# Kernel tuning notes

Hardware: AMD Instinct MI355X
Metric: run time of the kernel (lower is better)

Reference implementation:

```python
import jax, jax.numpy as jnp
import numpy as np

D = 256      # d_model
NH = 8       # num heads
L = 2        # encoder layers
FF = 512     # dim_feedforward
WS = 2       # HiLo window_size
HD = D // NH # head dim = 32
LH = 4       # lofi heads (alpha=0.5)
HH = 4       # hifi heads
LD = LH * HD # 128
HDIM = HH * HD  # 128
SCALE = HD ** -0.5


def _ln(x, g, b):
    m = jnp.mean(x, -1, keepdims=True)
    v = jnp.mean((x - m) ** 2, -1, keepdims=True)
    return (x - m) / jnp.sqrt(v + 1e-5) * g + b


def _hilo(x, H, Wlq, Wlkv, Wlp, blp, Whqkv, Whp, bhp):
    N, B, C = x.shape
    x = x.reshape(B, H, N // H, C)  # faithful to torch: pure reshape, no permute
    Bc, Hh, Ww, Cc = x.shape
    hg, wg = Hh // WS, Ww // WS
    tg, n = hg * wg, WS * WS
    # ---- hifi: local windowed attention ----
    xg = x.reshape(Bc, hg, WS, wg, WS, Cc).swapaxes(2, 3).reshape(Bc, tg, n, Cc)
    qkv = (xg @ Whqkv).reshape(Bc, tg, n, 3, HH, HD)
    qkv = jnp.transpose(qkv, (3, 0, 1, 4, 2, 5))  # (3, B, tg, heads, n, hd)
    q, k, v = qkv[0], qkv[1], qkv[2]
    a = jax.nn.softmax((q @ jnp.swapaxes(k, -2, -1)) * SCALE, axis=-1)
    o = (a @ v).swapaxes(2, 3).reshape(Bc, hg, wg, WS, WS, HDIM)
    o = o.swapaxes(2, 3).reshape(Bc, Hh, Ww, HDIM)
    hi = o @ Whp + bhp
    # ---- lofi: full queries vs avg-pooled kv ----
    q = (x @ Wlq).reshape(Bc, Hh * Ww, LH, HD).transpose(0, 2, 1, 3)
    xp = x.reshape(Bc, hg, WS, wg, WS, Cc).mean(axis=(2, 4)).reshape(Bc, tg, Cc)
    kv = (xp @ Wlkv).reshape(Bc, tg, 2, LH, HD).transpose(2, 0, 3, 1, 4)
    k, v = kv[0], kv[1]
    a = jax.nn.softmax((q @ jnp.swapaxes(k, -2, -1)) * SCALE, axis=-1)
    lo = (a @ v).swapaxes(1, 2).reshape(Bc, Hh, Ww, LD) @ Wlp + blp
    return jnp.concatenate([hi, lo], axis=-1).reshape(N, B, C)


def setup_inputs() -> dict:
    key = jax.random.key(0)
    ks = jax.random.split(key, 10)
    w = lambda k, s: jax.random.normal(k, s, jnp.float32) * 0.02
    N, B = 128, 1024
    return {
        "tgt": jax.random.normal(ks[0], (N, B, D), jnp.float32),
        "Wlq": w(ks[1], (L, D, LD)),
        "Wlkv": w(ks[2], (L, D, 2 * LD)),
        "Wlp": w(ks[3], (L, LD, LD)),
        "blp": jnp.zeros((L, LD), jnp.float32),
        "Whqkv": w(ks[4], (L, D, 3 * HDIM)),
        "Whp": w(ks[5], (L, HDIM, HDIM)),
        "bhp": jnp.zeros((L, HDIM), jnp.float32),
        "W1": w(ks[6], (L, D, FF)),
        "b1": jnp.zeros((L, FF), jnp.float32),
        "W2": w(ks[7], (L, FF, D)),
        "b2": jnp.zeros((L, D), jnp.float32),
        "ln1_g": jnp.ones((L, D), jnp.float32),
        "ln1_b": jnp.zeros((L, D), jnp.float32),
        "ln2_g": jnp.ones((L, D), jnp.float32),
        "ln2_b": jnp.zeros((L, D), jnp.float32),
        "lnf_g": jnp.ones((D,), jnp.float32),
        "lnf_b": jnp.zeros((D,), jnp.float32),
        "enc_win_h": 8,
    }


def reference(tgt, Wlq, Wlkv, Wlp, blp, Whqkv, Whp, bhp, W1, b1, W2, b2,
              ln1_g, ln1_b, ln2_g, ln2_b, lnf_g, lnf_b, enc_win_h):
    out = tgt
    for i in range(L):
        a = _hilo(out, enc_win_h, Wlq[i], Wlkv[i], Wlp[i], blp[i], Whqkv[i], Whp[i], bhp[i])
        out = _ln(out + a, ln1_g[i], ln1_b[i])
        f = jax.nn.relu(out @ W1[i] + b1[i]) @ W2[i] + b2[i]
        out = _ln(out + f, ln2_g[i], ln2_b[i])
    out = _ln(out, lnf_g, lnf_b)
    return out[None]  # (1, N, B, C), matching output.unsqueeze(0)
```

## Files before the change

kernel.cpp:

```cpp
#include <hip/hip_runtime.h>
#include <hip/hip_bf16.h>


#define RT 131072ull
#define ATT_SCALE 0.17677669529663687f

typedef float f32x4 __attribute__((ext_vector_type(4)));
typedef __bf16 bf16x8 __attribute__((ext_vector_type(8)));
typedef unsigned short u16x8 __attribute__((ext_vector_type(8)));
typedef unsigned short u16x4 __attribute__((ext_vector_type(4)));

__device__ __forceinline__ unsigned short f2bf(float f) {
    unsigned int u = __float_as_uint(f);
    return (unsigned short)((u + 0x7FFFu + ((u >> 16) & 1u)) >> 16);
}
__device__ __forceinline__ float bf2f(unsigned short s) {
    return __uint_as_float(((unsigned int)s) << 16);
}
__device__ __forceinline__ void gload16(const void* g, void* l) {
    __builtin_amdgcn_global_load_lds(
        (const __attribute__((address_space(1))) unsigned int*)g,
        (__attribute__((address_space(3))) unsigned int*)l, 16, 0, 0);
}

__global__ __launch_bounds__(256) void wprep(const float* __restrict__ src,
                                             unsigned short* __restrict__ dst,
                                             int K, int N)
{
    __shared__ unsigned short t[32][33];
    int l = blockIdx.z;
    const float* s = src + (size_t)l * K * N;
    unsigned short* d = dst + (size_t)l * K * N;
    int r = threadIdx.x >> 3, c4 = (threadIdx.x & 7) * 4;
    int kb = blockIdx.x * 32, nb = blockIdx.y * 32;
    f32x4 v = *(const f32x4*)(s + (size_t)(kb + r) * N + nb + c4);
    #pragma unroll
    for (int j = 0; j < 4; ++j) t[c4 + j][r] = f2bf(v[j]);
    __syncthreads();
    u16x4 o;
    #pragma unroll
    for (int j = 0; j < 4; ++j) o[j] = t[r][c4 + j];
    *(u16x4*)(d + (size_t)(nb + r) * K + kb + c4) = o;
}

__global__ __launch_bounds__(256) void cvt_bf16(const float* __restrict__ src,
                                                unsigned short* __restrict__ dst)
{
    size_t i = ((size_t)blockIdx.x * 256 + threadIdx.x) * 8;
    f32x4 a = *(const f32x4*)(src + i);
    f32x4 b = *(const f32x4*)(src + i + 4);
    u16x8 t;
    #pragma unroll
    for (int j = 0; j < 4; ++j) { t[j] = f2bf(a[j]); t[4 + j] = f2bf(b[j]); }
    *(u16x8*)(dst + i) = t;
}

template<int MT, int NT, int KS>
__device__ __forceinline__ void mfma_gemm(const char* As, int astride, int am0,
    const unsigned short* __restrict__ BT, int ldbk, int koff,
    int lr, int lk, f32x4 (&acc)[MT][NT])
{
    #pragma unroll
    for (int s = 0; s < KS; ++s) {
        bf16x8 bfr[NT];
        #pragma unroll
        for (int nt = 0; nt < NT; ++nt)
            bfr[nt] = *(const bf16x8*)(BT + (size_t)(nt * 16 + lr) * ldbk + koff + s * 32 + lk * 8);
        #pragma unroll
        for (int mt = 0; mt < MT; ++mt) {
            int row = am0 + mt * 16 + lr;
            bf16x8 afr = *(const bf16x8*)(As + ((row * astride + s * 64 + lk * 16) ^ ((row & 7) << 4)));
            #pragma unroll
            for (int nt = 0; nt < NT; ++nt)
                acc[mt][nt] = __builtin_amdgcn_mfma_f32_16x16x32_bf16(afr, bfr[nt], acc[mt][nt], 0, 0, 0);
        }
    }
}

template<int MT, int NT, bool RELU>
__device__ __forceinline__ void store_lds(char* Ds, int dstride, int dm0, int dn0,
    const float* bias, int lr, int lk, f32x4 (&acc)[MT][NT])
{
    #pragma unroll
    for (int nt = 0; nt < NT; ++nt) {
        float bv = bias ? bias[nt * 16 + lr] : 0.0f;
        #pragma unroll
        for (int mt = 0; mt < MT; ++mt) {
            #pragma unroll
            for (int j = 0; j < 4; ++j) {
                int row = dm0 + mt * 16 + lk * 4 + j;
                int col = dn0 + nt * 16 + lr;
                float v = acc[mt][nt][j] + bv;
                if (RELU) v = fmaxf(v, 0.0f);
                *(unsigned short*)(Ds + ((row * dstride + col * 2) ^ ((row & 7) << 4))) = f2bf(v);
            }
        }
    }
}

template<int BN, bool BIAS, bool RELU>
__global__ __launch_bounds__(256) void gemm_bb(
    const unsigned short* __restrict__ A, int lda,
    const unsigned short* __restrict__ BT,
    const float* __restrict__ bias,
    unsigned short* __restrict__ C, int ldc, int K)
{
    constexpr int NT = BN / 32;
    __shared__ __align__(16) char As[128 * 128];
    __shared__ __align__(16) char Bs[BN * 128];

    const int tid = threadIdx.x;
    const size_t m0 = (size_t)blockIdx.x * 128;
    const int n0 = blockIdx.y * BN;
    const int w = tid >> 6, l = tid & 63;
    const int lr = l & 15, lk = l >> 4;
    const int wm = w >> 1, wn = w & 1;
    const int wb16 = (tid & ~63) * 16;

    f32x4 acc[4][NT] = {};

    for (int k0 = 0; k0 < K; k0 += 64) {
        #pragma unroll
        for (int i = 0; i < 4; ++i) {
            int cid = tid + i * 256, row = cid >> 3, kc = (cid & 7) ^ (row & 7);
            gload16(A + (m0 + row) * lda + k0 + kc * 8, As + i * 4096 + wb16);
        }
        #pragma unroll
        for (int i = 0; i < BN / 32; ++i) {
            int fid = tid + i * 256, row = fid >> 3, kc = (fid & 7) ^ (row & 7);
            gload16(BT + (size_t)(n0 + row) * K + k0 + kc * 8, Bs + i * 4096 + wb16);
        }
        __syncthreads();
        #pragma unroll
        for (int s = 0; s < 2; ++s) {
            bf16x8 bfr[NT];
            #pragma unroll
            for (int nt = 0; nt < NT; ++nt) {
                int r = wn * (BN / 2) + nt * 16 + lr;
                bfr[nt] = *(const bf16x8*)(Bs + ((r * 128 + s * 64 + lk * 16) ^ ((r & 7) << 4)));
            }
            #pragma unroll
            for (int mt = 0; mt < 4; ++mt) {
                int r = wm * 64 + mt * 16 + lr;
                bf16x8 afr = *(const bf16x8*)(As + ((r * 128 + s * 64 + lk * 16) ^ ((r & 7) << 4)));
                #pragma unroll
                for (int nt = 0; nt < NT; ++nt)
                    acc[mt][nt] = __builtin_amdgcn_mfma_f32_16x16x32_bf16(afr, bfr[nt], acc[mt][nt], 0, 0, 0);
            }
        }
        __syncthreads();
    }
    #pragma unroll
    for (int nt = 0; nt < NT; ++nt) {
        int col = n0 + wn * (BN / 2) + nt * 16 + lr;
        float bv = BIAS ? bias[col] : 0.0f;
        #pragma unroll
        for (int mt = 0; mt < 4; ++mt) {
            #pragma unroll
            for (int j = 0; j < 4; ++j) {
                size_t row = m0 + (size_t)(wm * 64 + mt * 16 + lk * 4 + j);
                float v = acc[mt][nt][j] + bv;
                if (RELU) v = fmaxf(v, 0.0f);
                C[row * ldc + col] = f2bf(v);
            }
        }
    }
}

__global__ __launch_bounds__(256) void hilo_ln(
    const unsigned short* __restrict__ os,
    const unsigned short* __restrict__ los,
    const unsigned short* __restrict__ x,
    const unsigned short* __restrict__ tWhp,
    const unsigned short* __restrict__ tWlp,
    const float* __restrict__ bhp, const float* __restrict__ blp,
    const float* __restrict__ g, const float* __restrict__ b,
    unsigned short* __restrict__ xout)
{
    __shared__ __align__(16) char sb[32768];
    char* Ao = sb;
    char* Al = sb + 16384;

    const int tid = threadIdx.x;
    const int w = tid >> 6, l = tid & 63;
    const int lr = l & 15, lk = l >> 4;
    const int wb16 = (tid & ~63) * 16;
    const size_t r0 = (size_t)blockIdx.x * 64;

    #pragma unroll
    for (int i = 0; i < 4; ++i) {
        int cid = tid + i * 256, row = cid >> 4, kc = (cid & 15) ^ (row & 7);
        gload16(os + (r0 + row) * 128 + kc * 8, Ao + i * 4096 + wb16);
        gload16(los + (r0 + row) * 128 + kc * 8, Al + i * 4096 + wb16);
    }
    __syncthreads();

    {
        const char* At = (w < 2) ? Ao : Al;
        const unsigned short* BTw = (w < 2) ? tWhp + (size_t)(w * 64) * 128
                                            : tWlp + (size_t)((w - 2) * 64) * 128;
        const float* biasw = (w < 2) ? bhp + w * 64 : blp + (w - 2) * 64;
        f32x4 acc[4][4] = {};
        mfma_gemm<4, 4, 4>(At, 256, 0, BTw, 128, 0, lr, lk, acc);
        __syncthreads();
        store_lds<4, 4, false>(sb, 512, 0, w * 64, biasw, lr, lk, acc);
    }
    __syncthreads();

    {
        int lrow = tid >> 2, c0 = (tid & 3) * 64;
        int xo = lrow * 512, sw = (lrow & 7) << 4;
        const unsigned short* xp = x + (r0 + lrow) * 256 + c0;
        float v[64];
        #pragma unroll
        for (int c = 0; c < 8; ++c) {
            u16x8 tr = *(const u16x8*)(sb + ((xo + c0 * 2 + c * 16) ^ sw));
            u16x8 tx = *(const u16x8*)(xp + c * 8);
            #pragma unroll
            for (int j = 0; j < 8; ++j) v[c * 8 + j] = bf2f(tx[j]) + bf2f(tr[j]);
        }
        float s = 0.0f, sq = 0.0f;
        #pragma unroll
        for (int j = 0; j < 64; ++j) { s += v[j]; sq += v[j] * v[j]; }
        s += __shfl_xor(s, 1); s += __shfl_xor(s, 2);
        sq += __shfl_xor(sq, 1); sq += __shfl_xor(sq, 2);
        float mean = s * (1.0f / 256.0f);
        float rstd = rsqrtf(sq * (1.0f / 256.0f) - mean * mean + 1e-5f);
        unsigned short* op = xout + (r0 + lrow) * 256 + c0;
        #pragma unroll
        for (int c = 0; c < 8; ++c) {
            u16x8 t;
            #pragma unroll
            for (int j = 0; j < 8; ++j)
                t[j] = f2bf((v[c * 8 + j] - mean) * rstd * g[c0 + c * 8 + j] + b[c0 + c * 8 + j]);
            *(u16x8*)(op + c * 8) = t;
        }
    }
}

__global__ __launch_bounds__(256) void hifi_attn(const unsigned short* __restrict__ qkv,
                                                 unsigned short* __restrict__ os)
{
    int t = blockIdx.x * 256 + threadIdx.x;
    int wdw = t >> 4, h = (t >> 2) & 3, qi = t & 3;
    int bc = wdw >> 5, tw = wdw & 31;
    int rbase = bc * 128 + (tw >> 3) * 32 + (tw & 7) * 2;
    int qrow = rbase + ((qi >> 1) << 4) + (qi & 1);

    const unsigned short* qp = qkv + (size_t)qrow * 384 + h * 32;
    float q[32];
    #pragma unroll
    for (int c = 0; c < 4; ++c) {
        u16x8 v = *(const u16x8*)(qp + c * 8);
        #pragma unroll
        for (int j = 0; j < 8; ++j) q[c * 8 + j] = bf2f(v[j]);
    }
    float s4[4];
    #pragma unroll
    for (int j = 0; j < 4; ++j) {
        int kr = rbase + ((j >> 1) << 4) + (j & 1);
        const unsigned short* kp = qkv + (size_t)kr * 384 + 128 + h * 32;
        float d = 0.0f;
        #pragma unroll
        for (int c = 0; c < 4; ++c) {
            u16x8 v = *(const u16x8*)(kp + c * 8);
            #pragma unroll
            for (int jj = 0; jj < 8; ++jj) d += q[c * 8 + jj] * bf2f(v[jj]);
        }
        s4[j] = d * ATT_SCALE;
    }
    float mx = fmaxf(fmaxf(s4[0], s4[1]), fmaxf(s4[2], s4[3]));
    float den = 0.0f;
    #pragma unroll
    for (int j = 0; j < 4; ++j) { s4[j] = __expf(s4[j] - mx); den += s4[j]; }
    float inv = 1.0f / den;

    float o[32];
    #pragma unroll
    for (int i = 0; i < 32; ++i) o[i] = 0.0f;
    #pragma unroll
    for (int j = 0; j < 4; ++j) {
        int vr = rbase + ((j >> 1) << 4) + (j & 1);
        const unsigned short* vp = qkv + (size_t)vr * 384 + 256 + h * 32;
        float a = s4[j] * inv;
        #pragma unroll
        for (int c = 0; c < 4; ++c) {
            u16x8 v = *(const u16x8*)(vp + c * 8);
            #pragma unroll
            for (int jj = 0; jj < 8; ++jj) o[c * 8 + jj] += a * bf2f(v[jj]);
        }
    }
    unsigned short* op = os + (size_t)qrow * 128 + h * 32;
    #pragma unroll
    for (int c = 0; c < 4; ++c) {
        u16x8 v;
        #pragma unroll
        for (int j = 0; j < 8; ++j) v[j] = f2bf(o[c * 8 + j]);
        *(u16x8*)(op + c * 8) = v;
    }
}

__global__ __launch_bounds__(256) void pool_k(const unsigned short* __restrict__ x,
                                              unsigned short* __restrict__ xp)
{
    int id = blockIdx.x * 256 + threadIdx.x;
    int p = id >> 5, c8 = (id & 31) * 8;
    int bc = p >> 5, tw = p & 31;
    int rbase = bc * 128 + (tw >> 3) * 32 + (tw & 7) * 2;
    const unsigned short* x0 = x + (size_t)rbase * 256 + c8;
    float a[8] = {};
    const int offs[4] = {0, 256, 16 * 256, 17 * 256};
    #pragma unroll
    for (int r = 0; r < 4; ++r) {
        u16x8 v = *(const u16x8*)(x0 + offs[r]);
        #pragma unroll
        for (int j = 0; j < 8; ++j) a[j] += bf2f(v[j]);
    }
    u16x8 o;
    #pragma unroll
    for (int j = 0; j < 8; ++j) o[j] = f2bf(a[j] * 0.25f);
    *(u16x8*)(xp + (size_t)p * 256 + c8) = o;
}

__global__ __launch_bounds__(128) void lofi_attn(const unsigned short* __restrict__ qb,
                                                 const unsigned short* __restrict__ kvb,
                                                 unsigned short* __restrict__ ob)
{
    __shared__ float ks[32][36];
    __shared__ float vs[32][36];
    int bc = blockIdx.x >> 2, h = blockIdx.x & 3;
    int tid = threadIdx.x;

    #pragma unroll
    for (int i = 0; i < 2; ++i) {
        int fid = tid + i * 128;
        int row = fid >> 3, cc = (fid & 7) * 4;
        const unsigned short* kp = kvb + (size_t)(bc * 32 + row) * 256 + h * 32 + cc;
        u16x4 kk = *(const u16x4*)kp;
        u16x4 vv = *(const u16x4*)(kp + 128);
        #pragma unroll
        for (int j = 0; j < 4; ++j) { ks[row][cc + j] = bf2f(kk[j]); vs[row][cc + j] = bf2f(vv[j]); }
    }

    const unsigned short* qp = qb + (size_t)(bc * 128 + tid) * 128 + h * 32;
    float q[32];
    #pragma unroll
    for (int c = 0; c < 4; ++c) {
        u16x8 v = *(const u16x8*)(qp + c * 8);
        #pragma unroll
        for (int j = 0; j < 8; ++j) q[c * 8 + j] = bf2f(v[j]);
    }
    __syncthreads();

    float sc[32];
    #pragma unroll
    for (int tk = 0; tk < 32; ++tk) {
        float d = 0.0f;
        #pragma unroll
        for (int i = 0; i < 32; ++i) d += q[i] * ks[tk][i];
        sc[tk] = d * ATT_SCALE;
    }
    float mx = -1e30f;
    #pragma unroll
    for (int tk = 0; tk < 32; ++tk) mx = fmaxf(mx, sc[tk]);
    float den = 0.0f;
    #pragma unroll
    for (int tk = 0; tk < 32; ++tk) { sc[tk] = __expf(sc[tk] - mx); den += sc[tk]; }
    float inv = 1.0f / den;

    float o[32];
    #pragma unroll
    for (int i = 0; i < 32; ++i) o[i] = 0.0f;
    #pragma unroll
    for (int tk = 0; tk < 32; ++tk) {
        float a = sc[tk];
        #pragma unroll
        for (int i = 0; i < 32; ++i) o[i] += a * vs[tk][i];
    }
    unsigned short* op = ob + (size_t)(bc * 128 + tid) * 128 + h * 32;
    #pragma unroll
    for (int c = 0; c < 4; ++c) {
        u16x8 v;
        #pragma unroll
        for (int j = 0; j < 8; ++j) v[j] = f2bf(o[c * 8 + j] * inv);
        *(u16x8*)(op + c * 8) = v;
    }
}

template<int MODE>
__global__ __launch_bounds__(256) void addln(
    const unsigned short* __restrict__ x,
    const unsigned short* __restrict__ r1,
    const float* __restrict__ g, const float* __restrict__ b,
    const float* __restrict__ g2, const float* __restrict__ b2,
    unsigned short* __restrict__ xout, float* __restrict__ fout)
{
    size_t row = (size_t)blockIdx.x * 4 + (threadIdx.x >> 6);
    int l = threadIdx.x & 63;
    u16x4 xv = *(const u16x4*)(x + row * 256 + l * 4);
    u16x4 rv = *(const u16x4*)(r1 + row * 256 + l * 4);
    f32x4 v;
    #pragma unroll
    for (int j = 0; j < 4; ++j) v[j] = bf2f(xv[j]) + bf2f(rv[j]);
    float s = v[0] + v[1] + v[2] + v[3];
    float sq = v[0] * v[0] + v[1] * v[1] + v[2] * v[2] + v[3] * v[3];
    #pragma unroll
    for (int off = 32; off > 0; off >>= 1) { s += __shfl_xor(s, off); sq += __shfl_xor(sq, off); }
    float mean = s * (1.0f / 256.0f);
    float rstd = rsqrtf(sq * (1.0f / 256.0f) - mean * mean + 1e-5f);
    f32x4 gv = *(const f32x4*)(g + l * 4);
    f32x4 bv = *(const f32x4*)(b + l * 4);
    f32x4 o;
    #pragma unroll
    for (int j = 0; j < 4; ++j) o[j] = (v[j] - mean) * rstd * gv[j] + bv[j];
    if (MODE == 2) {
        float s2 = o[0] + o[1] + o[2] + o[3];
        float sq2 = o[0] * o[0] + o[1] * o[1] + o[2] * o[2] + o[3] * o[3];
        #pragma unroll
        for (int off = 32; off > 0; off >>= 1) { s2 += __shfl_xor(s2, off); sq2 += __shfl_xor(sq2, off); }
        float mean2 = s2 * (1.0f / 256.0f);
        float rstd2 = rsqrtf(sq2 * (1.0f / 256.0f) - mean2 * mean2 + 1e-5f);
        f32x4 g2v = *(const f32x4*)(g2 + l * 4);
        f32x4 b2v = *(const f32x4*)(b2 + l * 4);
        f32x4 f;
        #pragma unroll
        for (int j = 0; j < 4; ++j) f[j] = (o[j] - mean2) * rstd2 * g2v[j] + b2v[j];
        *(f32x4*)(fout + row * 256 + l * 4) = f;
    } else {
        u16x4 t;
        #pragma unroll
        for (int j = 0; j < 4; ++j) t[j] = f2bf(o[j]);
        *(u16x4*)(xout + row * 256 + l * 4) = t;
    }
}

extern "C" void kernel_launch(void* const* d_in, const int* in_sizes, int n_in,
                              void* d_out, int out_size, void* d_ws, size_t ws_size,
                              hipStream_t stream)
{
    (void)in_sizes; (void)n_in; (void)out_size; (void)ws_size;
    const float* tgt   = (const float*)d_in[0];
    const float* Wlq   = (const float*)d_in[1];
    const float* Wlkv  = (const float*)d_in[2];
    const float* Wlp   = (const float*)d_in[3];
    const float* blp   = (const float*)d_in[4];
    const float* Whqkv = (const float*)d_in[5];
    const float* Whp   = (const float*)d_in[6];
    const float* bhp   = (const float*)d_in[7];
    const float* W1    = (const float*)d_in[8];
    const float* b1    = (const float*)d_in[9];
    const float* W2    = (const float*)d_in[10];
    const float* b2    = (const float*)d_in[11];
    const float* ln1g  = (const float*)d_in[12];
    const float* ln1b  = (const float*)d_in[13];
    const float* ln2g  = (const float*)d_in[14];
    const float* ln2b  = (const float*)d_in[15];
    const float* lnfg  = (const float*)d_in[16];
    const float* lnfb  = (const float*)d_in[17];

    unsigned short* wsu = (unsigned short*)d_ws;
    unsigned short* tWhqkv = wsu;
    unsigned short* tWhp   = wsu + 196608;
    unsigned short* tWlq   = wsu + 229376;
    unsigned short* tWlkv  = wsu + 294912;
    unsigned short* tWlp   = wsu + 425984;
    unsigned short* tW1    = wsu + 458752;
    unsigned short* tW2    = wsu + 720896;
    unsigned short* x    = wsu + 983040;
    unsigned short* qkv  = x + RT * 256;
    unsigned short* f    = qkv;
    unsigned short* los  = qkv + RT * 256;
    unsigned short* os   = qkv + RT * 384;
    unsigned short* qb   = os;
    unsigned short* xp   = os + RT * 128;
    unsigned short* kv   = xp + 32768ull * 256;
    unsigned short* hbuf = kv + 32768ull * 256;

    wprep<<<dim3(8, 12, 2), 256, 0, stream>>>(Whqkv, tWhqkv, 256, 384);
    wprep<<<dim3(4,  4, 2), 256, 0, stream>>>(Whp,   tWhp,   128, 128);
    wprep<<<dim3(8,  4, 2), 256, 0, stream>>>(Wlq,   tWlq,   256, 128);
    wprep<<<dim3(8,  8, 2), 256, 0, stream>>>(Wlkv,  tWlkv,  256, 256);
    wprep<<<dim3(4,  4, 2), 256, 0, stream>>>(Wlp,   tWlp,   128, 128);
    wprep<<<dim3(8, 16, 2), 256, 0, stream>>>(W1,    tW1,    256, 512);
    wprep<<<dim3(16, 8, 2), 256, 0, stream>>>(W2,    tW2,    512, 256);

    cvt_bf16<<<16384, 256, 0, stream>>>(tgt, x);

    for (int li = 0; li < 2; ++li) {
        gemm_bb<128, false, false><<<dim3(1024, 3), 256, 0, stream>>>(
            x, 256, tWhqkv + (size_t)li * 98304, nullptr, qkv, 384, 256);
        hifi_attn<<<2048, 256, 0, stream>>>(qkv, os);
        gemm_bb<128, false, false><<<dim3(1024, 1), 256, 0, stream>>>(
            x, 256, tWlq + (size_t)li * 32768, nullptr, hbuf, 128, 256);
        pool_k<<<4096, 256, 0, stream>>>(x, xp);
        gemm_bb<128, false, false><<<dim3(256, 2), 256, 0, stream>>>(
            xp, 256, tWlkv + (size_t)li * 65536, nullptr, kv, 256, 256);
        lofi_attn<<<4096, 128, 0, stream>>>(hbuf, kv, los);
        hilo_ln<<<2048, 256, 0, stream>>>(
            os, los, x, tWhp + (size_t)li * 16384, tWlp + (size_t)li * 16384,
            bhp + li * 128, blp + li * 128, ln1g + li * 256, ln1b + li * 256, x);
        gemm_bb<128, true, true><<<dim3(1024, 4), 256, 0, stream>>>(
            x, 256, tW1 + (size_t)li * 131072, b1 + li * 512, hbuf, 512, 256);
        gemm_bb<128, true, false><<<dim3(1024, 2), 256, 0, stream>>>(
            hbuf, 512, tW2 + (size_t)li * 131072, b2 + li * 256, f, 256, 512);
        if (li == 0) {
            addln<1><<<32768, 256, 0, stream>>>(x, f, ln2g, ln2b,
                                                nullptr, nullptr, x, nullptr);
        } else {
            addln<2><<<32768, 256, 0, stream>>>(x, f, ln2g + 256, ln2b + 256,
                                                lnfg, lnfb, nullptr, (float*)d_out);
        }
    }
}
```

Before: 967.6 us.

## Double-buffer GEMM LDS tiles and fuse hifi QKV with lofi Q projection

Converts the bf16 GEMM to double-buffered LDS, issuing the next K-tile's async global-to-LDS loads before computing the current tile, so memory latency overlaps MFMA work. It also concatenates the Whqkv and Wlq weights into one 512-wide matrix, so a single GEMM produces both the hifi QKV and the lofi Q. The attention kernels then read from the wider 512-stride buffer. LDS use doubles, which may lower occupancy, and the buffer layout is reshuffled.

```diff
diff --git a/kernel.cpp b/kernel.cpp
--- a/kernel.cpp
+++ b/kernel.cpp
@@ -25,12 +25,12 @@
 
 __global__ __launch_bounds__(256) void wprep(const float* __restrict__ src,
                                              unsigned short* __restrict__ dst,
-                                             int K, int N)
+                                             int K, int N, int ldd)
 {
     __shared__ unsigned short t[32][33];
     int l = blockIdx.z;
     const float* s = src + (size_t)l * K * N;
-    unsigned short* d = dst + (size_t)l * K * N;
+    unsigned short* d = dst + (size_t)l * ldd;
     int r = threadIdx.x >> 3, c4 = (threadIdx.x & 7) * 4;
     int kb = blockIdx.x * 32, nb = blockIdx.y * 32;
     f32x4 v = *(const f32x4*)(s + (size_t)(kb + r) * N + nb + c4);
@@ -99,15 +99,15 @@
 }
 
 template<int BN, bool BIAS, bool RELU>
-__global__ __launch_bounds__(256) void gemm_bb(
+__global__ __launch_bounds__(256) void gemm_db(
     const unsigned short* __restrict__ A, int lda,
     const unsigned short* __restrict__ BT,
     const float* __restrict__ bias,
     unsigned short* __restrict__ C, int ldc, int K)
 {
     constexpr int NT = BN / 32;
-    __shared__ __align__(16) char As[128 * 128];
-    __shared__ __align__(16) char Bs[BN * 128];
+    __shared__ __align__(16) char As[2][128 * 128];
+    __shared__ __align__(16) char Bs[2][BN * 128];
 
     const int tid = threadIdx.x;
     const size_t m0 = (size_t)blockIdx.x * 128;
@@ -118,31 +118,39 @@
     const int wb16 = (tid & ~63) * 16;
 
     f32x4 acc[4][NT] = {};
-
-    for (int k0 = 0; k0 < K; k0 += 64) {
+    const int nk = K >> 6;
+
+    auto stage = [&](int b, int k0) {
         #pragma unroll
         for (int i = 0; i < 4; ++i) {
             int cid = tid + i * 256, row = cid >> 3, kc = (cid & 7) ^ (row & 7);
-            gload16(A + (m0 + row) * lda + k0 + kc * 8, As + i * 4096 + wb16);
+            gload16(A + (m0 + row) * lda + k0 + kc * 8, As[b] + i * 4096 + wb16);
         }
         #pragma unroll
         for (int i = 0; i < BN / 32; ++i) {
             int fid = tid + i * 256, row = fid >> 3, kc = (fid & 7) ^ (row & 7);
-            gload16(BT + (size_t)(n0 + row) * K + k0 + kc * 8, Bs + i * 4096 + wb16);
-        }
-        __syncthreads();
+            gload16(BT + (size_t)(n0 + row) * K + k0 + kc * 8, Bs[b] + i * 4096 + wb16);
+        }
+    };
+
+    stage(0, 0);
+    __syncthreads();
+    for (int t = 0; t < nk; ++t) {
+        if (t + 1 < nk) stage((t + 1) & 1, (t + 1) << 6);
+        const char* Ab = As[t & 1];
+        const char* Bb = Bs[t & 1];
         #pragma unroll
         for (int s = 0; s < 2; ++s) {
             bf16x8 bfr[NT];
             #pragma unroll
             for (int nt = 0; nt < NT; ++nt) {
                 int r = wn * (BN / 2) + nt * 16 + lr;
-                bfr[nt] = *(const bf16x8*)(Bs + ((r * 128 + s * 64 + lk * 16) ^ ((r & 7) << 4)));
+                bfr[nt] = *(const bf16x8*)(Bb + ((r * 128 + s * 64 + lk * 16) ^ ((r & 7) << 4)));
             }
             #pragma unroll
             for (int mt = 0; mt < 4; ++mt) {
                 int r = wm * 64 + mt * 16 + lr;
-                bf16x8 afr = *(const bf16x8*)(As + ((r * 128 + s * 64 + lk * 16) ^ ((r & 7) << 4)));
+                bf16x8 afr = *(const bf16x8*)(Ab + ((r * 128 + s * 64 + lk * 16) ^ ((r & 7) << 4)));
                 #pragma unroll
                 for (int nt = 0; nt < NT; ++nt)
                     acc[mt][nt] = __builtin_amdgcn_mfma_f32_16x16x32_bf16(afr, bfr[nt], acc[mt][nt], 0, 0, 0);
@@ -247,7 +255,7 @@
     int rbase = bc * 128 + (tw >> 3) * 32 + (tw & 7) * 2;
     int qrow = rbase + ((qi >> 1) << 4) + (qi & 1);
 
-    const unsigned short* qp = qkv + (size_t)qrow * 384 + h * 32;
+    const unsigned short* qp = qkv + (size_t)qrow * 512 + h * 32;
     float q[32];
     #pragma unroll
     for (int c = 0; c < 4; ++c) {
@@ -259,7 +267,7 @@
     #pragma unroll
     for (int j = 0; j < 4; ++j) {
         int kr = rbase + ((j >> 1) << 4) + (j & 1);
-        const unsigned short* kp = qkv + (size_t)kr * 384 + 128 + h * 32;
+        const unsigned short* kp = qkv + (size_t)kr * 512 + 128 + h * 32;
         float d = 0.0f;
         #pragma unroll
         for (int c = 0; c < 4; ++c) {
@@ -281,7 +289,7 @@
     #pragma unroll
     for (int j = 0; j < 4; ++j) {
         int vr = rbase + ((j >> 1) << 4) + (j & 1);
-        const unsigned short* vp = qkv + (size_t)vr * 384 + 256 + h * 32;
+        const unsigned short* vp = qkv + (size_t)vr * 512 + 256 + h * 32;
         float a = s4[j] * inv;
         #pragma unroll
         for (int c = 0; c < 4; ++c) {
@@ -323,6 +331,7 @@
 }
 
 __global__ __launch_bounds__(128) void lofi_attn(const unsigned short* __restrict__ qb,
+                                                 int ldq,
                                                  const unsigned short* __restrict__ kvb,
                                                  unsigned short* __restrict__ ob)
 {
@@ -342,7 +351,7 @@
         for (int j = 0; j < 4; ++j) { ks[row][cc + j] = bf2f(kk[j]); vs[row][cc + j] = bf2f(vv[j]); }
     }
 
-    const unsigned short* qp = qb + (size_t)(bc * 128 + tid) * 128 + h * 32;
+    const unsigned short* qp = qb + (size_t)(bc * 128 + tid) * ldq + h * 32;
     float q[32];
     #pragma unroll
     for (int c = 0; c < 4; ++c) {
@@ -459,49 +468,45 @@
     const float* lnfb  = (const float*)d_in[17];
 
     unsigned short* wsu = (unsigned short*)d_ws;
-    unsigned short* tWhqkv = wsu;
-    unsigned short* tWhp   = wsu + 196608;
-    unsigned short* tWlq   = wsu + 229376;
+    unsigned short* tQ     = wsu;
+    unsigned short* tWhp   = wsu + 262144;
     unsigned short* tWlkv  = wsu + 294912;
     unsigned short* tWlp   = wsu + 425984;
     unsigned short* tW1    = wsu + 458752;
     unsigned short* tW2    = wsu + 720896;
-    unsigned short* x    = wsu + 983040;
-    unsigned short* qkv  = x + RT * 256;
-    unsigned short* f    = qkv;
-    unsigned short* los  = qkv + RT * 256;
-    unsigned short* os   = qkv + RT * 384;
-    unsigned short* qb   = os;
-    unsigned short* xp   = os + RT * 128;
-    unsigned short* kv   = xp + 32768ull * 256;
-    unsigned short* hbuf = kv + 32768ull * 256;
-
-    wprep<<<dim3(8, 12, 2), 256, 0, stream>>>(Whqkv, tWhqkv, 256, 384);
-    wprep<<<dim3(4,  4, 2), 256, 0, stream>>>(Whp,   tWhp,   128, 128);
-    wprep<<<dim3(8,  4, 2), 256, 0, stream>>>(Wlq,   tWlq,   256, 128);
-    wprep<<<dim3(8,  8, 2), 256, 0, stream>>>(Wlkv,  tWlkv,  256, 256);
-    wprep<<<dim3(4,  4, 2), 256, 0, stream>>>(Wlp,   tWlp,   128, 128);
-    wprep<<<dim3(8, 16, 2), 256, 0, stream>>>(W1,    tW1,    256, 512);
-    wprep<<<dim3(16, 8, 2), 256, 0, stream>>>(W2,    tW2,    512, 256);
+    unsigned short* x      = wsu + 983040;
+    unsigned short* qkv2   = x + RT * 256;
+    unsigned short* f      = qkv2;
+    unsigned short* xp     = qkv2 + RT * 512;
+    unsigned short* kv     = xp + 32768ull * 256;
+    unsigned short* hbuf   = kv + 32768ull * 256;
+    unsigned short* los    = hbuf;
+    unsigned short* os     = hbuf + RT * 128;
+
+    wprep<<<dim3(8, 12, 2), 256, 0, stream>>>(Whqkv, tQ, 256, 384, 131072);
+    wprep<<<dim3(8,  4, 2), 256, 0, stream>>>(Wlq, tQ + 98304, 256, 128, 131072);
+    wprep<<<dim3(4,  4, 2), 256, 0, stream>>>(Whp,  tWhp,  128, 128, 16384);
+    wprep<<<dim3(8,  8, 2), 256, 0, stream>>>(Wlkv, tWlkv, 256, 256, 65536);
+    wprep<<<dim3(4,  4, 2), 256, 0, stream>>>(Wlp,  tWlp,  128, 128, 16384);
+    wprep<<<dim3(8, 16, 2), 256, 0, stream>>>(W1,   tW1,   256, 512, 131072);
+    wprep<<<dim3(16, 8, 2), 256, 0, stream>>>(W2,   tW2,   512, 256, 131072);
 
     cvt_bf16<<<16384, 256, 0, stream>>>(tgt, x);
 
     for (int li = 0; li < 2; ++li) {
-        gemm_bb<128, false, false><<<dim3(1024, 3), 256, 0, stream>>>(
-            x, 256, tWhqkv + (size_t)li * 98304, nullptr, qkv, 384, 256);
-        hifi_attn<<<2048, 256, 0, stream>>>(qkv, os);
-        gemm_bb<128, false, false><<<dim3(1024, 1), 256, 0, stream>>>(
-            x, 256, tWlq + (size_t)li * 32768, nullptr, hbuf, 128, 256);
+        gemm_db<128, false, false><<<dim3(1024, 4), 256, 0, stream>>>(
+            x, 256, tQ + (size_t)li * 131072, nullptr, qkv2, 512, 256);
+        hifi_attn<<<2048, 256, 0, stream>>>(qkv2, os);
         pool_k<<<4096, 256, 0, stream>>>(x, xp);
-        gemm_bb<128, false, false><<<dim3(256, 2), 256, 0, stream>>>(
+        gemm_db<128, false, false><<<dim3(256, 2), 256, 0, stream>>>(
             xp, 256, tWlkv + (size_t)li * 65536, nullptr, kv, 256, 256);
-        lofi_attn<<<4096, 128, 0, stream>>>(hbuf, kv, los);
+        lofi_attn<<<4096, 128, 0, stream>>>(qkv2 + 384, 512, kv, los);
         hilo_ln<<<2048, 256, 0, stream>>>(
             os, los, x, tWhp + (size_t)li * 16384, tWlp + (size_t)li * 16384,
             bhp + li * 128, blp + li * 128, ln1g + li * 256, ln1b + li * 256, x);
-        gemm_bb<128, true, true><<<dim3(1024, 4), 256, 0, stream>>>(
+        gemm_db<128, true, true><<<dim3(1024, 4), 256, 0, stream>>>(
             x, 256, tW1 + (size_t)li * 131072, b1 + li * 512, hbuf, 512, 256);
-        gemm_bb<128, true, false><<<dim3(1024, 2), 256, 0, stream>>>(
+        gemm_db<128, true, false><<<dim3(1024, 2), 256, 0, stream>>>(
             hbuf, 512, tW2 + (size_t)li * 131072, b2 + li * 256, f, 256, 512);
         if (li == 0) {
             addln<1><<<32768, 256, 0, stream>>>(x, f, ln2g, ln2b,
```

Result: no change. 964.9 us (-0.3%).
